# Kernel tuning notes

Measured on AMD Instinct MI355X. Metric: run time of the kernel, lower is better.

The kernel has to match this reference:

```python
import jax, jax.numpy as jnp
import numpy as np

B, H, W = 64, 512, 512          # batch, image height/width
BH, BW = 8, 8                   # block_size
K = 256                         # n_blocks (codebook size)
L = BH * BW                     # block_len = 64
HT, WT = H // BH, W // BW       # tiles per axis
T = HT * WT                     # tiles_per_img = 4096
BETA = 35.0


def _unfold(img):
    # img: (B, 1, H, W) -> patches (B, T, L), matching torch.nn.Unfold
    # with kernel=stride=(BH,BW): tiles row-major, patch flattened (kh, kw).
    x = img.reshape(B, 1, HT, BH, WT, BW)
    x = x.transpose(0, 2, 4, 1, 3, 5)          # (B, HT, WT, 1, BH, BW)
    return x.reshape(B, T, L)


def _fold(patches):
    # patches: (B, T, L) -> img (B, 1, H, W); exact inverse of _unfold
    # (non-overlapping, so Fold is pure reassembly, no accumulation).
    x = patches.reshape(B, HT, WT, 1, BH, BW)
    x = x.transpose(0, 3, 1, 4, 2, 5)          # (B, 1, HT, BH, WT, BW)
    return x.reshape(B, 1, H, W)


def setup_inputs() -> dict:
    key = jax.random.key(0)
    k1, k2 = jax.random.split(key)
    target_img = jax.random.uniform(k1, (B, 1, H, W), dtype=jnp.float32)
    # Learned codebook parameter (Haar-ish init in the original; values
    # don't change the math being tested).
    blocks = jax.random.uniform(k2, (K, BH, BW), dtype=jnp.float32)
    return {"target_img": target_img, "blocks": blocks}


def reference(target_img, blocks):
    patches = _unfold(target_img).reshape(B * T, L)   # (N, L), N = B*T
    codes = blocks.reshape(K, L)                      # (K, L)

    # Squared distances ||a - b||^2 via the expanded form to avoid
    # materializing the (N, K, L) difference tensor.
    a2 = jnp.sum(patches * patches, axis=-1, keepdims=True)   # (N, 1)
    b2 = jnp.sum(codes * codes, axis=-1)                      # (K,)
    ab = patches @ codes.T                                    # (N, K)
    sqerr = a2 - 2.0 * ab + b2                                # (N, K)

    block_weights = jax.nn.softmax(-BETA * sqerr, axis=-1)    # (N, K)
    uf_reconstructed = block_weights @ codes                  # (N, L)

    reconstructed = _fold(uf_reconstructed.reshape(B, T, L))  # (B,1,H,W)
    choice_penalty = jnp.mean(
        jnp.minimum(block_weights, 1.0 - block_weights)) * K
    return reconstructed, choice_penalty
```

## Files before the change

### kernel.cpp

```cpp
#include <hip/hip_runtime.h>


typedef short short8 __attribute__((ext_vector_type(8)));
typedef float floatx4 __attribute__((ext_vector_type(4)));

namespace {
constexpr float BETA_C = 35.0f;
constexpr float TAU    = 1e-6f;
constexpr float INV_N  = 1.0f / 262144.0f;
constexpr size_t IMG_ELEMS = (size_t)64 * 512 * 512;
constexpr int WB0 = 0;
constexpr int WB1 = 4096;
constexpr int WR  = 0;
constexpr int WS  = 4352;
constexpr int NWORDS = 8192;
}

__device__ __forceinline__ unsigned short f2bf(float x) {
  unsigned u = __float_as_uint(x);
  return (unsigned short)((u + 0x7FFFu + ((u >> 16) & 1u)) >> 16);
}
__device__ __forceinline__ float bf2f(unsigned short h) {
  return __uint_as_float((unsigned)h << 16);
}
__device__ __forceinline__ unsigned pack2(unsigned short lo, unsigned short hi) {
  return (unsigned)lo | ((unsigned)hi << 16);
}
__device__ __forceinline__ void cvt8t(float4 a, float4 b, short8& h, short8& l) {
  float f[8] = {a.x, a.y, a.z, a.w, b.x, b.y, b.z, b.w};
#pragma unroll
  for (int i = 0; i < 8; ++i) {
    unsigned short hh = f2bf(f[i]);
    h[i] = (short)hh;
    float lf = f[i] - bf2f(hh);
    l[i] = (short)(__float_as_uint(lf) >> 16);
  }
}
__device__ __forceinline__ void cp16(const uint4* g, unsigned* l) {
  __builtin_amdgcn_global_load_lds(
      (const __attribute__((address_space(1))) void*)g,
      (__attribute__((address_space(3))) void*)l, 16, 0, 0);
}

__global__ void pack_codes(const float* __restrict__ blk,
                           unsigned* __restrict__ wsBh,
                           unsigned* __restrict__ wsBl,
                           float* __restrict__ wsB2) {
  const int gid = blockIdx.x * 256 + threadIdx.x;
  const int c = gid >> 3, g = gid & 7;
  const float* src = blk + c * 64 + g * 8;
  float4 a = *reinterpret_cast<const float4*>(src);
  float4 b = *reinterpret_cast<const float4*>(src + 4);
  float f[8] = {a.x, a.y, a.z, a.w, b.x, b.y, b.z, b.w};
  uint4 ph, pl;
  unsigned* phw = reinterpret_cast<unsigned*>(&ph);
  unsigned* plw = reinterpret_cast<unsigned*>(&pl);
  float b2 = 0.f;
#pragma unroll
  for (int t = 0; t < 4; ++t) {
    float v0 = f[2 * t], v1 = f[2 * t + 1];
    b2 += v0 * v0 + v1 * v1;
    unsigned short h0 = f2bf(v0), h1 = f2bf(v1);
    unsigned short l0 = f2bf(v0 - bf2f(h0)), l1 = f2bf(v1 - bf2f(h1));
    phw[t] = pack2(h0, h1);
    plw[t] = pack2(l0, l1);
  }
  const int slot = c * 8 + (g ^ (c & 7));
  reinterpret_cast<uint4*>(wsBh)[slot] = ph;
  reinterpret_cast<uint4*>(wsBl)[slot] = pl;
  b2 += __shfl_xor(b2, 1, 64);
  b2 += __shfl_xor(b2, 2, 64);
  b2 += __shfl_xor(b2, 4, 64);
  if (g == 0) wsB2[c] = -BETA_C * b2;
}

__global__ __launch_bounds__(256, 4) void recon_kernel(
    const float* __restrict__ img, const float* __restrict__ blk,
    const unsigned* __restrict__ wsBh, const unsigned* __restrict__ wsBl,
    const float* __restrict__ wsB2, float* __restrict__ out,
    float* __restrict__ penAcc) {
  __shared__ unsigned sMem[NWORDS];
  float* sMemF = reinterpret_cast<float*>(sMem);

  const int tid = threadIdx.x;
  const int lane = tid & 63;
  const int wave = tid >> 6;
  const int b = blockIdx.x >> 6;
  const int ht = blockIdx.x & 63;
  const int c15 = lane & 15;
  const int q = lane >> 4;

  const float* imgBase = img + (size_t)b * (512 * 512) + (size_t)(ht * 8) * 512;
  const float* aptr = imgBase + q * 512 + (wave * 16 + c15) * 8;
  float4 v00 = *reinterpret_cast<const float4*>(aptr);
  float4 v01 = *reinterpret_cast<const float4*>(aptr + 4);
  float4 v10 = *reinterpret_cast<const float4*>(aptr + 2048);
  float4 v11 = *reinterpret_cast<const float4*>(aptr + 2048 + 4);

  const uint4* srcH = reinterpret_cast<const uint4*>(wsBh);
  const uint4* srcL = reinterpret_cast<const uint4*>(wsBl);
#pragma unroll
  for (int i = 0; i < 4; ++i) {
    cp16(srcH + i * 256 + tid, &sMem[WB0 + (i * 4 + wave) * 256]);
    cp16(srcL + i * 256 + tid, &sMem[WB1 + (i * 4 + wave) * 256]);
  }

  short8 ah[2], al[2];
  cvt8t(v00, v01, ah[0], al[0]);
  cvt8t(v10, v11, ah[1], al[1]);

  asm volatile("s_waitcnt vmcnt(0)" ::: "memory");
  __syncthreads();

  const int kx = c15 & 7;
  const unsigned* pb0 = &sMem[(8 * c15 + (q ^ kx)) * 4];
  const unsigned* pb1 = &sMem[(8 * c15 + ((q ^ 4) ^ kx)) * 4];

  float m[4], sm[4];
  float rr[16] = {0.f, 0.f, 0.f, 0.f, 0.f, 0.f, 0.f, 0.f,
                  0.f, 0.f, 0.f, 0.f, 0.f, 0.f, 0.f, 0.f};

#pragma unroll
  for (int h = 0; h < 2; ++h) {
    floatx4 acc[8];
#pragma unroll
    for (int n = 0; n < 8; ++n) acc[n] = (floatx4){0.f, 0.f, 0.f, 0.f};
#pragma unroll
    for (int n = 0; n < 8; ++n) {
      short8 b0h = *reinterpret_cast<const short8*>(pb0 + 512 * n);
      short8 b1h = *reinterpret_cast<const short8*>(pb1 + 512 * n);
      short8 b0l = *reinterpret_cast<const short8*>(pb0 + WB1 + 512 * n);
      short8 b1l = *reinterpret_cast<const short8*>(pb1 + WB1 + 512 * n);
      acc[n] = __builtin_amdgcn_mfma_f32_16x16x32_bf16(ah[0], b0h, acc[n], 0, 0, 0);
      acc[n] = __builtin_amdgcn_mfma_f32_16x16x32_bf16(al[0], b0h, acc[n], 0, 0, 0);
      acc[n] = __builtin_amdgcn_mfma_f32_16x16x32_bf16(ah[1], b1h, acc[n], 0, 0, 0);
      acc[n] = __builtin_amdgcn_mfma_f32_16x16x32_bf16(al[1], b1h, acc[n], 0, 0, 0);
      acc[n] = __builtin_amdgcn_mfma_f32_16x16x32_bf16(ah[0], b0l, acc[n], 0, 0, 0);
      acc[n] = __builtin_amdgcn_mfma_f32_16x16x32_bf16(ah[1], b1l, acc[n], 0, 0, 0);
    }
    if (h == 0) {
      __syncthreads();
#pragma unroll
      for (int i = 0; i < 4; ++i) {
        cp16(srcH + 1024 + i * 256 + tid, &sMem[WB0 + (i * 4 + wave) * 256]);
        cp16(srcL + 1024 + i * 256 + tid, &sMem[WB1 + (i * 4 + wave) * 256]);
      }
    }

#pragma unroll
    for (int n = 0; n < 8; ++n) {
      float b2s = wsB2[128 * h + 16 * n + c15];
#pragma unroll
      for (int r = 0; r < 4; ++r)
        acc[n][r] = fmaf(2.0f * BETA_C, acc[n][r], b2s);
    }
    float M[4];
#pragma unroll
    for (int r = 0; r < 4; ++r) {
      float mm = acc[0][r];
#pragma unroll
      for (int n = 1; n < 8; ++n) mm = fmaxf(mm, acc[n][r]);
#pragma unroll
      for (int off = 1; off <= 8; off <<= 1) mm = fmaxf(mm, __shfl_xor(mm, off, 64));
      M[r] = mm;
    }
    if (h == 0) {
#pragma unroll
      for (int r = 0; r < 4; ++r) { m[r] = M[r]; sm[r] = 0.f; }
    } else {
      float scl[4];
#pragma unroll
      for (int r = 0; r < 4; ++r) {
        float mn = fmaxf(m[r], M[r]);
        scl[r] = __expf(m[r] - mn);
        m[r] = mn;
        sm[r] *= scl[r];
      }
      bool moved = (scl[0] < 1.f) | (scl[1] < 1.f) | (scl[2] < 1.f) | (scl[3] < 1.f);
      if (__any(moved)) {
#pragma unroll
        for (int qq = 0; qq < 4; ++qq)
#pragma unroll
          for (int r = 0; r < 4; ++r) {
            float sq = __shfl(scl[r], qq * 16 + c15, 64);
            rr[4 * qq + r] *= sq;
          }
      }
    }
#pragma unroll
    for (int n = 0; n < 8; ++n)
#pragma unroll
      for (int r = 0; r < 4; ++r) {
        float e = __expf(acc[n][r] - m[r]);
        acc[n][r] = e;
        sm[r] += e;
      }
#pragma unroll
    for (int n = 0; n < 8; ++n) {
      float em = fmaxf(fmaxf(acc[n][0], acc[n][1]), fmaxf(acc[n][2], acc[n][3]));
      unsigned long long msk = __ballot(em > TAU);
      while (msk) {
        int L = __builtin_ctzll(msk);
        msk &= msk - 1;
        float w0 = __uint_as_float(__builtin_amdgcn_readlane(__float_as_uint(acc[n][0]), L));
        float w1 = __uint_as_float(__builtin_amdgcn_readlane(__float_as_uint(acc[n][1]), L));
        float w2 = __uint_as_float(__builtin_amdgcn_readlane(__float_as_uint(acc[n][2]), L));
        float w3 = __uint_as_float(__builtin_amdgcn_readlane(__float_as_uint(acc[n][3]), L));
        float bv = blk[(size_t)(128 * h + 16 * n + (L & 15)) * 64 + lane];
        switch (L >> 4) {
          case 0: rr[0] += w0 * bv;  rr[1] += w1 * bv;  rr[2] += w2 * bv;  rr[3] += w3 * bv;  break;
          case 1: rr[4] += w0 * bv;  rr[5] += w1 * bv;  rr[6] += w2 * bv;  rr[7] += w3 * bv;  break;
          case 2: rr[8] += w0 * bv;  rr[9] += w1 * bv;  rr[10] += w2 * bv; rr[11] += w3 * bv; break;
          default: rr[12] += w0 * bv; rr[13] += w1 * bv; rr[14] += w2 * bv; rr[15] += w3 * bv; break;
        }
      }
    }
    if (h == 0) {
      asm volatile("s_waitcnt vmcnt(0)" ::: "memory");
      __syncthreads();
    }
  }

  float invS[4];
#pragma unroll
  for (int r = 0; r < 4; ++r) {
#pragma unroll
    for (int off = 1; off <= 8; off <<= 1) sm[r] += __shfl_xor(sm[r], off, 64);
    invS[r] = 1.0f / sm[r];
  }
  float pen = 0.f;
  if (c15 == 0) {
#pragma unroll
    for (int r = 0; r < 4; ++r)
      pen += (invS[r] > 0.5f) ? (2.0f - 2.0f * invS[r]) : 1.0f;
  }
  pen += __shfl_xor(pen, 16, 64);
  pen += __shfl_xor(pen, 32, 64);
  if (lane == 0) atomicAdd(penAcc, pen * INV_N);

  __syncthreads();

  if (c15 == 0) {
#pragma unroll
    for (int r = 0; r < 4; ++r)
      sMemF[WS + wave * 16 + 4 * q + r] = invS[r];
  }
#pragma unroll
  for (int pl = 0; pl < 16; ++pl)
    sMemF[WR + (wave * 16 + pl) * 68 + lane] = rr[pl];
  float* outBase = out + (size_t)b * (512 * 512) + (size_t)(ht * 8) * 512 +
                   wave * 128;
#pragma unroll
  for (int i = 0; i < 4; ++i) {
    int f = i * 64 + lane;
    int row = f >> 5;
    int cc = f & 31;
    int wtl = cc >> 1, hw = cc & 1;
    float4 v = *reinterpret_cast<const float4*>(
        &sMemF[WR + (wave * 16 + wtl) * 68 + row * 8 + hw * 4]);
    float is = sMemF[WS + wave * 16 + wtl];
    v.x *= is; v.y *= is; v.z *= is; v.w *= is;
    *reinterpret_cast<float4*>(outBase + row * 512 + cc * 4) = v;
  }
}

extern "C" void kernel_launch(void* const* d_in, const int* in_sizes, int n_in,
                              void* d_out, int out_size, void* d_ws, size_t ws_size,
                              hipStream_t stream) {
  const float* img = (const float*)d_in[0];
  const float* blk = (const float*)d_in[1];
  float* out = (float*)d_out;
  float* penSlot = out + IMG_ELEMS;

  unsigned* wsBh = (unsigned*)d_ws;
  unsigned* wsBl = wsBh + 8192;
  float* wsB2 = (float*)(wsBl + 8192);

  pack_codes<<<dim3(8), dim3(256), 0, stream>>>(blk, wsBh, wsBl, wsB2);
  hipMemsetAsync(penSlot, 0, sizeof(float), stream);
  recon_kernel<<<dim3(4096), dim3(256), 0, stream>>>(img, blk, wsBh, wsBl,
                                                     wsB2, out, penSlot);
}
```

Measured before the change: 326.4 us.

## Split reconstruction into sparse weight-list stash and separate gather kernel

The fused kernel no longer accumulates the reconstruction with ballot/readlane loops. It now records, per patch, a capped list (24 slots) of significant codebook entries, each as an fp16 logit delta plus a code index, using LDS atomics. The normalized weights are written as a scratch stash into the output image strip. A second kernel reads each list, gathers codebook rows and writes the final image. This is meant to cut the serialized per-lane loop and register pressure, at the cost of an extra launch, global round-trip traffic and precision/truncation risk (fp16 deltas, entries dropped beyond 24 slots).

After: 408.4 us. 25.2% more time.

```diff
diff --git a/kernel.cpp b/kernel.cpp
--- a/kernel.cpp
+++ b/kernel.cpp
@@ -1,4 +1,5 @@
 #include <hip/hip_runtime.h>
+#include <hip/hip_fp16.h>
 
 
 typedef short short8 __attribute__((ext_vector_type(8)));
@@ -9,11 +10,12 @@
 constexpr float TAU    = 1e-6f;
 constexpr float INV_N  = 1.0f / 262144.0f;
 constexpr size_t IMG_ELEMS = (size_t)64 * 512 * 512;
+constexpr int NSLOT = 24;
 constexpr int WB0 = 0;
 constexpr int WB1 = 4096;
-constexpr int WR  = 0;
-constexpr int WS  = 4352;
-constexpr int NWORDS = 8192;
+constexpr int WP  = 8192;
+constexpr int WC  = 9728;
+constexpr int NWORDS = 9792;
 }
 
 __device__ __forceinline__ unsigned short f2bf(float x) {
@@ -75,12 +77,11 @@
 }
 
 __global__ __launch_bounds__(256, 4) void recon_kernel(
-    const float* __restrict__ img, const float* __restrict__ blk,
+    const float* __restrict__ img,
     const unsigned* __restrict__ wsBh, const unsigned* __restrict__ wsBl,
-    const float* __restrict__ wsB2, float* __restrict__ out,
-    float* __restrict__ penAcc) {
+    const float* __restrict__ wsB2,
+    float* __restrict__ out, float* __restrict__ penAcc) {
   __shared__ unsigned sMem[NWORDS];
-  float* sMemF = reinterpret_cast<float*>(sMem);
 
   const int tid = threadIdx.x;
   const int lane = tid & 63;
@@ -90,6 +91,8 @@
   const int c15 = lane & 15;
   const int q = lane >> 4;
 
+  if (lane < 16) sMem[WC + wave * 16 + lane] = 0;
+
   const float* imgBase = img + (size_t)b * (512 * 512) + (size_t)(ht * 8) * 512;
   const float* aptr = imgBase + q * 512 + (wave * 16 + c15) * 8;
   float4 v00 = *reinterpret_cast<const float4*>(aptr);
@@ -116,9 +119,7 @@
   const unsigned* pb0 = &sMem[(8 * c15 + (q ^ kx)) * 4];
   const unsigned* pb1 = &sMem[(8 * c15 + ((q ^ 4) ^ kx)) * 4];
 
-  float m[4], sm[4];
-  float rr[16] = {0.f, 0.f, 0.f, 0.f, 0.f, 0.f, 0.f, 0.f,
-                  0.f, 0.f, 0.f, 0.f, 0.f, 0.f, 0.f, 0.f};
+  float m[4], mOld[4], sm[4];
 
 #pragma unroll
   for (int h = 0; h < 2; ++h) {
@@ -168,53 +169,31 @@
 #pragma unroll
       for (int r = 0; r < 4; ++r) { m[r] = M[r]; sm[r] = 0.f; }
     } else {
-      float scl[4];
 #pragma unroll
       for (int r = 0; r < 4; ++r) {
+        mOld[r] = m[r];
         float mn = fmaxf(m[r], M[r]);
-        scl[r] = __expf(m[r] - mn);
+        sm[r] *= __expf(m[r] - mn);
         m[r] = mn;
-        sm[r] *= scl[r];
       }
-      bool moved = (scl[0] < 1.f) | (scl[1] < 1.f) | (scl[2] < 1.f) | (scl[3] < 1.f);
-      if (__any(moved)) {
-#pragma unroll
-        for (int qq = 0; qq < 4; ++qq)
-#pragma unroll
-          for (int r = 0; r < 4; ++r) {
-            float sq = __shfl(scl[r], qq * 16 + c15, 64);
-            rr[4 * qq + r] *= sq;
+    }
+#pragma unroll
+    for (int n = 0; n < 8; ++n)
+#pragma unroll
+      for (int r = 0; r < 4; ++r) {
+        float d = acc[n][r] - m[r];
+        float e = __expf(d);
+        sm[r] += e;
+        if (e > TAU) {
+          int p16 = wave * 16 + 4 * q + r;
+          unsigned idx = atomicAdd(&sMem[WC + p16], 1u);
+          if (idx < (unsigned)NSLOT) {
+            unsigned db = (unsigned)__half_as_ushort(__float2half(d));
+            sMem[WP + p16 * NSLOT + idx] =
+                (db << 16) | (unsigned)(128 * h + 16 * n + c15);
           }
-      }
-    }
-#pragma unroll
-    for (int n = 0; n < 8; ++n)
-#pragma unroll
-      for (int r = 0; r < 4; ++r) {
-        float e = __expf(acc[n][r] - m[r]);
-        acc[n][r] = e;
-        sm[r] += e;
-      }
-#pragma unroll
-    for (int n = 0; n < 8; ++n) {
-      float em = fmaxf(fmaxf(acc[n][0], acc[n][1]), fmaxf(acc[n][2], acc[n][3]));
-      unsigned long long msk = __ballot(em > TAU);
-      while (msk) {
-        int L = __builtin_ctzll(msk);
-        msk &= msk - 1;
-        float w0 = __uint_as_float(__builtin_amdgcn_readlane(__float_as_uint(acc[n][0]), L));
-        float w1 = __uint_as_float(__builtin_amdgcn_readlane(__float_as_uint(acc[n][1]), L));
-        float w2 = __uint_as_float(__builtin_amdgcn_readlane(__float_as_uint(acc[n][2]), L));
-        float w3 = __uint_as_float(__builtin_amdgcn_readlane(__float_as_uint(acc[n][3]), L));
-        float bv = blk[(size_t)(128 * h + 16 * n + (L & 15)) * 64 + lane];
-        switch (L >> 4) {
-          case 0: rr[0] += w0 * bv;  rr[1] += w1 * bv;  rr[2] += w2 * bv;  rr[3] += w3 * bv;  break;
-          case 1: rr[4] += w0 * bv;  rr[5] += w1 * bv;  rr[6] += w2 * bv;  rr[7] += w3 * bv;  break;
-          case 2: rr[8] += w0 * bv;  rr[9] += w1 * bv;  rr[10] += w2 * bv; rr[11] += w3 * bv; break;
-          default: rr[12] += w0 * bv; rr[13] += w1 * bv; rr[14] += w2 * bv; rr[15] += w3 * bv; break;
         }
       }
-    }
     if (h == 0) {
       asm volatile("s_waitcnt vmcnt(0)" ::: "memory");
       __syncthreads();
@@ -238,18 +217,56 @@
   pen += __shfl_xor(pen, 32, 64);
   if (lane == 0) atomicAdd(penAcc, pen * INV_N);
 
-  __syncthreads();
-
-  if (c15 == 0) {
-#pragma unroll
-    for (int r = 0; r < 4; ++r)
-      sMemF[WS + wave * 16 + 4 * q + r] = invS[r];
-  }
-#pragma unroll
-  for (int pl = 0; pl < 16; ++pl)
-    sMemF[WR + (wave * 16 + pl) * 68 + lane] = rr[pl];
-  float* outBase = out + (size_t)b * (512 * 512) + (size_t)(ht * 8) * 512 +
-                   wave * 128;
+  float* strip = out + (size_t)b * (512 * 512) + (size_t)(ht * 8) * 512;
+#pragma unroll
+  for (int pl = 0; pl < 16; ++pl) {
+    int rI = pl & 3, qI = pl >> 2;
+    float mo  = __shfl(mOld[rI], qI * 16, 64);
+    float mf  = __shfl(m[rI],    qI * 16, 64);
+    float isp = __shfl(invS[rI], qI * 16, 64);
+    int p16 = wave * 16 + pl;
+    unsigned cnt = sMem[WC + p16];
+    cnt = cnt > (unsigned)NSLOT ? (unsigned)NSLOT : cnt;
+    float* stash = strip + p16 * 8;
+    if (lane == 0) *reinterpret_cast<unsigned*>(stash + 6 * 512) = cnt;
+    if ((unsigned)lane < cnt) {
+      unsigned pw = sMem[WP + p16 * NSLOT + lane];
+      unsigned code = pw & 0xFFFFu;
+      float delta = __half2float(__ushort_as_half((unsigned short)(pw >> 16)));
+      float w = __expf(delta + (code < 128u ? mo - mf : 0.f)) * isp;
+      *reinterpret_cast<uint2*>(stash + (lane >> 2) * 512 + (lane & 3) * 2) =
+          make_uint2(__float_as_uint(w), code);
+    }
+  }
+}
+
+__global__ __launch_bounds__(256, 8) void recon2(const float* __restrict__ blk,
+                                                 float* __restrict__ out) {
+  __shared__ float sMemF[64 * 68];
+
+  const int tid = threadIdx.x;
+  const int lane = tid & 63;
+  const int wave = tid >> 6;
+  const int b = blockIdx.x >> 6;
+  const int ht = blockIdx.x & 63;
+
+  float* strip = out + (size_t)b * (512 * 512) + (size_t)(ht * 8) * 512;
+#pragma unroll
+  for (int pl = 0; pl < 16; ++pl) {
+    int p = wave * 16 + pl;
+    const float* stash = strip + p * 8;
+    unsigned cnt = *reinterpret_cast<const unsigned*>(stash + 6 * 512);
+    cnt = cnt > (unsigned)NSLOT ? (unsigned)NSLOT : cnt;
+    float rr = 0.f;
+    for (unsigned i = 0; i < cnt; ++i) {
+      uint2 pr = *reinterpret_cast<const uint2*>(
+          stash + (i >> 2) * 512 + (i & 3) * 2);
+      rr = fmaf(__uint_as_float(pr.x),
+                blk[(size_t)pr.y * 64 + lane], rr);
+    }
+    sMemF[p * 68 + lane] = rr;
+  }
+  float* outBase = strip + wave * 128;
 #pragma unroll
   for (int i = 0; i < 4; ++i) {
     int f = i * 64 + lane;
@@ -257,9 +274,7 @@
     int cc = f & 31;
     int wtl = cc >> 1, hw = cc & 1;
     float4 v = *reinterpret_cast<const float4*>(
-        &sMemF[WR + (wave * 16 + wtl) * 68 + row * 8 + hw * 4]);
-    float is = sMemF[WS + wave * 16 + wtl];
-    v.x *= is; v.y *= is; v.z *= is; v.w *= is;
+        &sMemF[(wave * 16 + wtl) * 68 + row * 8 + hw * 4]);
     *reinterpret_cast<float4*>(outBase + row * 512 + cc * 4) = v;
   }
 }
@@ -278,6 +293,7 @@
 
   pack_codes<<<dim3(8), dim3(256), 0, stream>>>(blk, wsBh, wsBl, wsB2);
   hipMemsetAsync(penSlot, 0, sizeof(float), stream);
-  recon_kernel<<<dim3(4096), dim3(256), 0, stream>>>(img, blk, wsBh, wsBl,
-                                                     wsB2, out, penSlot);
-}
+  recon_kernel<<<dim3(4096), dim3(256), 0, stream>>>(img, wsBh, wsBl, wsB2,
+                                                     out, penSlot);
+  recon2<<<dim3(4096), dim3(256), 0, stream>>>(blk, out);
+}
```
